# Optimization experiments

Hardware: AMD Instinct MI355X
Metric: run time of the kernel (lower is better)

The kernel has to match this reference:

```python
import jax, jax.numpy as jnp
import numpy as np

# ---- module hyperparameters (from init_kwargs) ----
J = 6      # number of octaves -> subsample by 2**J
Q = 6      # wavelets per octave
T = 16000  # signal length
SUB = 2 ** J           # downsampling factor (=> T_out = 250)
XI_MAX = 0.35          # max center frequency (cycles/sample), kymatio convention


def _build_filters(T, J, Q):
    """Gabor (Morlet-style) band-pass filterbank + Gaussian lowpass, in Fourier domain."""
    freqs = np.fft.fftfreq(T).astype(np.float64)          # (T,) cycles/sample
    n_psi = J * Q
    xis = XI_MAX * 2.0 ** (-np.arange(n_psi) / Q)         # constant-Q center freqs
    r = 2.0 ** (1.0 / Q)
    sigmas = xis * (r - 1.0) / (r + 1.0)                  # constant-Q bandwidths
    psi_hat = np.exp(-((freqs[None, :] - xis[:, None]) ** 2)
                     / (2.0 * sigmas[:, None] ** 2))       # (n_psi, T)
    sigma_phi = XI_MAX / (2.0 ** J)                        # lowpass bandwidth ~ 2^-J
    phi_hat = np.exp(-(freqs ** 2) / (2.0 * sigma_phi ** 2))  # (T,)
    return jnp.asarray(psi_hat, jnp.float32), jnp.asarray(phi_hat, jnp.float32)

PSI_HAT, PHI_HAT = _build_filters(T, J, Q)  # fixed (non-learned) filter constants


def setup_inputs() -> dict:
    key = jax.random.key(0)
    x = jax.random.normal(key, (64, 1, T), dtype=jnp.float32)
    return {"x": x}


def _scattering(x2d):
    """First-order scattering. x2d: (B, T) -> Sx: (B, 1 + J*Q, T//2**J)."""
    X = jnp.fft.fft(x2d, axis=-1)                                   # (B, T) complex
    # order 0: lowpass + subsample
    S0 = jnp.real(jnp.fft.ifft(X * PHI_HAT, axis=-1))[:, ::SUB]     # (B, T')
    # order 1: bandpass -> modulus -> lowpass -> subsample (vectorized over filters)
    U = jnp.abs(jnp.fft.ifft(X[:, None, :] * PSI_HAT[None, :, :], axis=-1))  # (B,JQ,T)
    S1 = jnp.real(jnp.fft.ifft(jnp.fft.fft(U, axis=-1) * PHI_HAT, axis=-1))[:, :, ::SUB]
    return jnp.concatenate([S0[:, None, :], S1], axis=1)            # (B, C, T')


def reference(x):
    # accept (B, T) or (B, 1, T) like the torch module
    if x.ndim == 3:
        x = x[:, 0, :]
    Sx = _scattering(x)[..., None]                                  # (B, C, T', 1)
    C = Sx.shape[1]
    c1 = max(1, C // 3)
    c2 = max(1, 2 * C // 3)
    low = Sx[:, :c1].mean(axis=1)
    mid = Sx[:, c1:c2].mean(axis=1)
    high = Sx[:, c2:].mean(axis=1)
    return jnp.stack([low, mid, high], axis=1)                      # (B, 3, T', 1)
```

## Files before the change

### kernel.cpp

```cpp
#include <hip/hip_runtime.h>
#include <hip/hip_bf16.h>
#include <hip/hip_fp16.h>

#define TLEN 16000
#define NPSI 36
#define NBATCH 64
#define NOUT 250
#define NCH 37
#define DHALF 176
#define KMAX 8000
#define TWO_PI 6.283185307179586

__device__ __forceinline__ int brev7(int q){ return (int)(__brev((unsigned)q) >> 25); }
__device__ __forceinline__ int drev125(int p){
    return (p % 5) * 25 + ((p / 5) % 5) * 5 + (p / 25);
}
__device__ __forceinline__ float lo2f(__half2 v){ return __low2float(v); }
__device__ __forceinline__ float hi2f(__half2 v){ return __high2float(v); }
__device__ __forceinline__ __half2 pk2(float r, float i){
    return __halves2half2(__float2half(r), __float2half(i));
}

__global__ __launch_bounds__(256) void k_ffta(const float* __restrict__ x,
                                              float2* __restrict__ Gtmp){
    __shared__ float xr[16 * 126], xi[16 * 126];
    __shared__ float w125r[125], w125i[125];
    __shared__ float w16r[125],  w16i[125];
    __shared__ float w128r[128], w128i[128];
    const int b = blockIdx.x >> 3, g = blockIdx.x & 7, row0 = 16 * g;
    const int tid = threadIdx.x;

    for (int j = tid; j < 125; j += 256){
        double a = -TWO_PI * (double)j / 125.0;
        w125r[j] = (float)cos(a); w125i[j] = (float)sin(a);
        double a2 = -TWO_PI * (double)j / 16000.0;
        w16r[j] = (float)cos(a2); w16i[j] = (float)sin(a2);
    }
    for (int j = tid; j < 128; j += 256){
        double a = -TWO_PI * (double)j / 128.0;
        w128r[j] = (float)cos(a); w128i[j] = (float)sin(a);
    }
    for (int i = tid; i < 16 * 125; i += 256){
        int n1 = i >> 4, lr = i & 15;
        xr[lr * 126 + n1] = x[b * TLEN + 128 * n1 + row0 + lr];
        xi[lr * 126 + n1] = 0.0f;
    }
    int f = 1;
    for (int s = 25; s >= 1; s /= 5, f *= 5){
        __syncthreads();
        for (int task = tid; task < 25 * 16; task += 256){
            int u = task >> 4, lr = task & 15;
            int blk = u / s, m = u - blk * s;
            int base = lr * 126 + blk * 5 * s + m;
            float vr[5], vi[5];
            #pragma unroll
            for (int r = 0; r < 5; ++r){ vr[r] = xr[base + r * s]; vi[r] = xi[base + r * s]; }
            #pragma unroll
            for (int q = 0; q < 5; ++q){
                float cr = vr[0], ci = vi[0];
                #pragma unroll
                for (int r = 1; r < 5; ++r){
                    int w5 = 25 * ((q * r) % 5);
                    float wr = w125r[w5], wi = w125i[w5];
                    cr += vr[r] * wr - vi[r] * wi;
                    ci += vr[r] * wi + vi[r] * wr;
                }
                int jt = (m * q * f) % 125;
                float tr = w125r[jt], ti = w125i[jt];
                xr[base + q * s] = cr * tr - ci * ti;
                xi[base + q * s] = cr * ti + ci * tr;
            }
        }
    }
    __syncthreads();
    for (int i = tid; i < 125 * 16; i += 256){
        int p = i >> 4, lr = i & 15;
        int n2 = row0 + lr;
        int m = drev125(p);
        int a = m * n2;
        int qq = a / 125, rr = a - qq * 125;
        float tr = w16r[rr] * w128r[qq] - w16i[rr] * w128i[qq];
        float ti = w16r[rr] * w128i[qq] + w16i[rr] * w128r[qq];
        float ar = xr[lr * 126 + p], ai = xi[lr * 126 + p];
        Gtmp[((size_t)b * 125 + p) * 128 + n2] =
            make_float2(ar * tr - ai * ti, ar * ti + ai * tr);
    }
}

__global__ __launch_bounds__(128) void k_fftb(const float2* __restrict__ Gtmp,
                                              float2* __restrict__ Xf){
    __shared__ float gr[128 * 5], gi[128 * 5];
    __shared__ float w128r[128], w128i[128];
    const int b = blockIdx.x / 25, p0 = (blockIdx.x % 25) * 5;
    const int tid = threadIdx.x;
    for (int j = tid; j < 128; j += 128){
        double a = -TWO_PI * (double)j / 128.0;
        w128r[j] = (float)cos(a); w128i[j] = (float)sin(a);
    }
    for (int i = tid; i < 5 * 128; i += 128){
        int ml = i >> 7, n2 = i & 127;
        float2 v = Gtmp[((size_t)b * 125 + p0 + ml) * 128 + n2];
        gr[n2 * 5 + ml] = v.x; gi[n2 * 5 + ml] = v.y;
    }
    for (int span = 64; span >= 1; span >>= 1){
        __syncthreads();
        for (int idx = tid; idx < 320; idx += 128){
            int u = idx / 5, ml = idx - u * 5;
            int blkq = u / span, mm = u % span;
            int i0 = (blkq * 2 * span + mm) * 5 + ml, i1 = i0 + span * 5;
            float ar = gr[i0], ai = gi[i0], br = gr[i1], bi = gi[i1];
            gr[i0] = ar + br; gi[i0] = ai + bi;
            float dr = ar - br, di = ai - bi;
            int jt = mm * (64 / span);
            gr[i1] = dr * w128r[jt] - di * w128i[jt];
            gi[i1] = dr * w128i[jt] + di * w128r[jt];
        }
    }
    __syncthreads();
    for (int idx = tid; idx < 320; idx += 128){
        int u = idx / 5, ml = idx - u * 5;
        int ad = (2 * u) * 5 + ml;
        int k = drev125(p0 + ml) + 125 * brev7(2 * u);
        Xf[(size_t)b * KMAX + k] = make_float2(gr[ad], gi[ad]);
    }
}

template<int P5, int LQ>
__device__ __forceinline__ void env_body(const float2* __restrict__ Xfb,
                                         float* __restrict__ Schan,
                                         int fi, int b, int tid,
                                         __half2* Bc,
                                         float* wPr, float* wPi,
                                         float* wNr, float* wNi,
                                         float* wQr, float* wQi,
                                         float* w5tr, float* w5ti,
                                         float* hfull, int* drevT, float* sred){
    constexpr int Q = 1 << LQ;
    constexpr int N = P5 * Q;
    constexpr int D = TLEN / N;
    constexpr int S1 = P5 / 5;
    constexpr int EPT = (LQ & 1) ? 2 : 4;
    constexpr int NTASK = N / EPT;
    constexpr int NFP = (NTASK + 511) / 512;
    __half* Mag = reinterpret_cast<__half*>(Bc);

    const double xi_d = 0.35 * exp2(-(double)fi / 6.0);
    const double r_d  = exp2(1.0 / 6.0);
    const double sig_d = xi_d * (r_d - 1.0) / (r_d + 1.0);
    const float xi = (float)xi_d;
    const float centerT = (float)(xi_d * (double)TLEN);
    const float sigT = (float)(sig_d * (double)TLEN);
    int klo = (int)floorf(centerT - 5.0f * sigT); if (klo < 1) klo = 1;
    int khi = (int)ceilf(centerT + 5.0f * sigT);  if (khi > KMAX - 1) khi = KMAX - 1;
    const float inv2s2 = (float)(1.0 / (2.0 * sig_d * sig_d));

    for (int j = tid; j < P5; j += 512){
        double a = TWO_PI * (double)j / (double)P5;
        wPr[j] = (float)cos(a); wPi[j] = (float)sin(a);
        double a2 = TWO_PI * (double)j / (double)N;
        wNr[j] = (float)cos(a2); wNi[j] = (float)sin(a2);
        drevT[j] = (P5 == 125) ? drev125(j) : ((j % 5) * 5 + j / 5);
    }
    for (int j = tid; j < Q; j += 512){
        double a = TWO_PI * (double)j / (double)Q;
        wQr[j] = (float)cos(a); wQi[j] = (float)sin(a);
    }
    for (int j = tid; j < 25; j += 512){
        double a = TWO_PI * (double)(((j / 5) * (j % 5)) % 5) / 5.0;
        w5tr[j] = (float)cos(a); w5ti[j] = (float)sin(a);
    }
    for (int j = tid; j <= 2 * DHALF; j += 512){
        double st = 1.0 / (TWO_PI * (0.35 / 64.0));
        double dd = (double)(j - DHALF);
        hfull[j] = (float)((0.35 / 64.0) * sqrt(TWO_PI) * exp(-0.5 * dd * dd / (st * st)));
    }
    __syncthreads();
    for (int task = tid; task < S1 * Q; task += 512){
        int m = task >> LQ, k2 = task & (Q - 1);
        float vr[5], vi[5];
        #pragma unroll
        for (int r = 0; r < 5; ++r){
            int gk = k2 + ((m + r * S1) << LQ);
            float ur = 0.0f, ui = 0.0f;
            if (gk >= klo && gk <= khi){
                float fr = (float)gk * (1.0f / (float)TLEN);
                float d = fr - xi;
                float p = __expf(-d * d * inv2s2) * (1.0f / (float)TLEN);
                float2 Xv = Xfb[gk];
                ur = Xv.x * p; ui = Xv.y * p;
            }
            vr[r] = ur; vi[r] = ui;
        }
        int base = m * Q + k2;
        #pragma unroll
        for (int q = 0; q < 5; ++q){
            float cr = vr[0], ci = vi[0];
            #pragma unroll
            for (int r = 1; r < 5; ++r){
                float wr = w5tr[q * 5 + r], wi = w5ti[q * 5 + r];
                cr += vr[r] * wr - vi[r] * wi;
                ci += vr[r] * wi + vi[r] * wr;
            }
            int jt = m * q;
            float tr = wPr[jt], ti = wPi[jt];
            Bc[base + q * S1 * Q] = pk2(cr * tr - ci * ti, cr * ti + ci * tr);
        }
    }
    if (P5 == 125){
        __syncthreads();
        for (int task = tid; task < 25 * Q; task += 512){
            int u = task >> LQ, k2 = task & (Q - 1);
            int blk = u / 5, m = u - blk * 5;
            int base = (blk * 25 + m) * Q + k2;
            float vr[5], vi[5];
            #pragma unroll
            for (int r = 0; r < 5; ++r){
                __half2 v = Bc[base + r * 5 * Q];
                vr[r] = lo2f(v); vi[r] = hi2f(v);
            }
            #pragma unroll
            for (int q = 0; q < 5; ++q){
                float cr = vr[0], ci = vi[0];
                #pragma unroll
                for (int r = 1; r < 5; ++r){
                    float wr = w5tr[q * 5 + r], wi = w5ti[q * 5 + r];
                    cr += vr[r] * wr - vi[r] * wi;
                    ci += vr[r] * wi + vi[r] * wr;
                }
                int jt = m * q * 5;
                float tr = wPr[jt], ti = wPi[jt];
                Bc[base + q * 5 * Q] = pk2(cr * tr - ci * ti, cr * ti + ci * tr);
            }
        }
    }
    __syncthreads();
    for (int task = tid; task < S1 * Q; task += 512){
        int u = task >> LQ, k2 = task & (Q - 1);
        int base = (u * 5) * Q + k2;
        float vr[5], vi[5];
        #pragma unroll
        for (int r = 0; r < 5; ++r){
            __half2 v = Bc[base + r * Q];
            vr[r] = lo2f(v); vi[r] = hi2f(v);
        }
        #pragma unroll
        for (int q = 0; q < 5; ++q){
            float cr = vr[0], ci = vi[0];
            #pragma unroll
            for (int r = 1; r < 5; ++r){
                float wr = w5tr[q * 5 + r], wi = w5ti[q * 5 + r];
                cr += vr[r] * wr - vi[r] * wi;
                ci += vr[r] * wi + vi[r] * wr;
            }
            int n1 = drevT[5 * u + q];
            int a = k2 * n1;
            int qq = a / P5, rr = a - qq * P5;
            float tr = wQr[qq] * wNr[rr] - wQi[qq] * wNi[rr];
            float ti = wQr[qq] * wNi[rr] + wQi[qq] * wNr[rr];
            Bc[base + q * Q] = pk2(cr * tr - ci * ti, cr * ti + ci * tr);
        }
    }
    #pragma unroll
    for (int pass = 0; pass + 1 < LQ / 2 + (LQ & 1); ++pass){
        const int Sp = Q >> (1 + 2 * pass);
        const int half = Sp >> 1;
        __syncthreads();
        for (int task = tid; task < P5 * (Q / 4); task += 512){
            int prow = task / (Q / 4), v = task & (Q / 4 - 1);
            int blkq = v / half, m = v - blkq * half;
            int base = prow * Q + blkq * 2 * Sp + m;
            __half2 vA = Bc[base],        vB = Bc[base + half];
            __half2 vC = Bc[base + Sp],   vD = Bc[base + Sp + half];
            float Ar = lo2f(vA), Ai = hi2f(vA);
            float B2r = lo2f(vB), B2i = hi2f(vB);
            float Cr = lo2f(vC), Ci = hi2f(vC);
            float D2r = lo2f(vD), D2i = hi2f(vD);
            int jt1 = m * ((Q / 2) / Sp);
            float w1r = wQr[jt1], w1i = wQi[jt1];
            float w2r = wQr[2 * jt1], w2i = wQi[2 * jt1];
            float A1r = Ar + Cr, A1i = Ai + Ci;
            float t1r = Ar - Cr, t1i = Ai - Ci;
            float C1r = t1r * w1r - t1i * w1i, C1i = t1r * w1i + t1i * w1r;
            float B1r = B2r + D2r, B1i = B2i + D2i;
            float t2r = B2r - D2r, t2i = B2i - D2i;
            float t3r = -t2i, t3i = t2r;
            float D1r = t3r * w1r - t3i * w1i, D1i = t3r * w1i + t3i * w1r;
            Bc[base] = pk2(A1r + B1r, A1i + B1i);
            float u1r = A1r - B1r, u1i = A1i - B1i;
            Bc[base + half] = pk2(u1r * w2r - u1i * w2i, u1r * w2i + u1i * w2r);
            Bc[base + Sp] = pk2(C1r + D1r, C1i + D1i);
            float u2r = C1r - D1r, u2i = C1i - D1i;
            Bc[base + Sp + half] = pk2(u2r * w2r - u2i * w2i, u2r * w2i + u2i * w2r);
        }
    }
    __syncthreads();
    float magf[NFP][EPT];
    #pragma unroll
    for (int i = 0; i < NFP; ++i){
        int task = tid + 512 * i;
        if (task < NTASK){
            if (LQ & 1){
                int p = task / (Q / 2), u = task - p * (Q / 2);
                int i0 = p * Q + 2 * u;
                __half2 v0 = Bc[i0], v1 = Bc[i0 + 1];
                float ar = lo2f(v0), ai = hi2f(v0);
                float br2 = lo2f(v1), bi2 = hi2f(v1);
                float o0r = ar + br2, o0i = ai + bi2;
                float o1r = ar - br2, o1i = ai - bi2;
                magf[i][0] = sqrtf(o0r * o0r + o0i * o0i);
                magf[i][1] = sqrtf(o1r * o1r + o1i * o1i);
            } else {
                int prow = task / (Q / 4), v = task & (Q / 4 - 1);
                int base = prow * Q + 4 * v;
                __half2 v0 = Bc[base], v1 = Bc[base + 1];
                __half2 v2 = Bc[base + 2], v3 = Bc[base + 3];
                float Ar = lo2f(v0), Ai = hi2f(v0);
                float B2r = lo2f(v1), B2i = hi2f(v1);
                float Cr = lo2f(v2), Ci = hi2f(v2);
                float D2r = lo2f(v3), D2i = hi2f(v3);
                float A1r = Ar + Cr, A1i = Ai + Ci;
                float C1r = Ar - Cr, C1i = Ai - Ci;
                float B1r = B2r + D2r, B1i = B2i + D2i;
                float t2r = B2r - D2r, t2i = B2i - D2i;
                float D1r = -t2i, D1i = t2r;
                float o0r = A1r + B1r, o0i = A1i + B1i;
                float o1r = A1r - B1r, o1i = A1i - B1i;
                float o2r = C1r + D1r, o2i = C1i + D1i;
                float o3r = C1r - D1r, o3i = C1i - D1i;
                magf[i][0] = sqrtf(o0r * o0r + o0i * o0i);
                magf[i][1] = sqrtf(o1r * o1r + o1i * o1i);
                magf[i][2] = sqrtf(o2r * o2r + o2i * o2i);
                magf[i][3] = sqrtf(o3r * o3r + o3i * o3i);
            }
        }
    }
    __syncthreads();
    #pragma unroll
    for (int i = 0; i < NFP; ++i){
        int task = tid + 512 * i;
        if (task < NTASK){
            int row, s0;
            if (LQ & 1){ row = task / (Q / 2); s0 = 2 * (task - row * (Q / 2)); }
            else       { row = task / (Q / 4); s0 = 4 * (task & (Q / 4 - 1)); }
            #pragma unroll
            for (int e = 0; e < EPT; ++e){
                int slot = s0 + e;
                int n2 = (int)(__brev((unsigned)slot) >> (32 - LQ));
                int np = drevT[row] + P5 * n2;
                Mag[np + (np >> 4)] = __float2half(magf[i][e]);
            }
        }
    }
    __syncthreads();
    float acc = 0.0f;
    if (tid < 500){
        int t = tid - 250 * (tid / 250);
        int q = tid / 250;
        int m0 = 64 * t;
        int lo = m0 - DHALF;
        int nlo = (lo >= 0) ? ((lo + D - 1) / D) : -((-lo) / D);
        int nhi = (m0 + DHALF) / D;
        int n = nlo + q;
        if (n <= nhi){
            int np = n % N; if (np < 0) np += N;
            int d = m0 - D * n + DHALF;
            for (; n <= nhi; n += 2){
                acc += hfull[d] * __half2float(Mag[np + (np >> 4)]);
                d -= 2 * D;
                np += 2; if (np >= N) np -= N;
            }
        }
        sred[tid] = acc;
    }
    __syncthreads();
    if (tid < 250)
        Schan[(b * NCH + 1 + fi) * NOUT + tid] = (sred[tid] + sred[tid + 250]) * (float)D;
}

__global__ __launch_bounds__(512, 4) void k_env_all(const float* __restrict__ x,
                                                    const float2* __restrict__ Xf,
                                                    float* __restrict__ Schan){
    __shared__ __half2 Bc[8000];
    __shared__ float wPr[125], wPi[125];
    __shared__ float wNr[125], wNi[125];
    __shared__ float wQr[128], wQi[128];
    __shared__ float w5tr[25], w5ti[25];
    __shared__ float hfull[2 * DHALF + 1];
    __shared__ int   drevT[125];
    __shared__ float sred[500];

    const int bi = blockIdx.x;
    const int tid = threadIdx.x;
    if (bi < 448){
        int fi = bi >> 6, b = bi & 63;
        env_body<125, 6>(Xf + (size_t)b * KMAX, Schan, fi, b, tid, Bc,
                         wPr, wPi, wNr, wNi, wQr, wQi, w5tr, w5ti, hfull, drevT, sred);
    } else if (bi < 640){
        int t = bi - 448;
        int fi = 7 + (t >> 6), b = t & 63;
        env_body<125, 5>(Xf + (size_t)b * KMAX, Schan, fi, b, tid, Bc,
                         wPr, wPi, wNr, wNi, wQr, wQi, w5tr, w5ti, hfull, drevT, sred);
    } else if (bi < 1088){
        int t = bi - 640;
        int fi = 10 + (t >> 6), b = t & 63;
        env_body<25, 7>(Xf + (size_t)b * KMAX, Schan, fi, b, tid, Bc,
                        wPr, wPi, wNr, wNi, wQr, wQi, w5tr, w5ti, hfull, drevT, sred);
    } else if (bi < 1408){
        int t = bi - 1088;
        int fi = 17 + (t >> 6), b = t & 63;
        env_body<125, 4>(Xf + (size_t)b * KMAX, Schan, fi, b, tid, Bc,
                         wPr, wPi, wNr, wNi, wQr, wQi, w5tr, w5ti, hfull, drevT, sred);
    } else if (bi < 2304){
        int t = bi - 1408;
        int fi = 22 + (t >> 6), b = t & 63;
        env_body<25, 6>(Xf + (size_t)b * KMAX, Schan, fi, b, tid, Bc,
                        wPr, wPi, wNr, wNi, wQr, wQi, w5tr, w5ti, hfull, drevT, sred);
    } else {
        int b = bi - 2304;
        const float* xb = x + (size_t)b * TLEN;
        for (int j = tid; j <= 2 * DHALF; j += 512){
            double st = 1.0 / (TWO_PI * (0.35 / 64.0));
            double dd = (double)(j - DHALF);
            hfull[j] = (float)((0.35 / 64.0) * sqrt(TWO_PI) * exp(-0.5 * dd * dd / (st * st)));
        }
        __syncthreads();
        float acc = 0.0f;
        if (tid < 500){
            int t = tid - 250 * (tid / 250);
            int q = tid / 250;
            int m0 = 64 * t;
            for (int j = q; j <= 2 * DHALF; j += 2){
                int n = m0 - DHALF + j;
                if (n < 0) n += TLEN; else if (n >= TLEN) n -= TLEN;
                acc += hfull[j] * xb[n];
            }
            sred[tid] = acc;
        }
        __syncthreads();
        if (tid < 250)
            Schan[(b * NCH + 0) * NOUT + tid] = sred[tid] + sred[tid + 250];
    }
}

__global__ __launch_bounds__(256) void k_reduce(const float* __restrict__ Schan,
                                                float* __restrict__ out){
    int o = blockIdx.x * 256 + threadIdx.x;
    if (o >= NBATCH * 3 * NOUT) return;
    int b = o / (3 * NOUT);
    int rem = o - b * 3 * NOUT;
    int g = rem / NOUT;
    int t = rem - g * NOUT;
    int c0 = (g == 0) ? 0 : (g == 1 ? 12 : 24);
    int c1 = (g == 0) ? 12 : (g == 1 ? 24 : 37);
    float s = 0.0f;
    for (int c = c0; c < c1; ++c) s += Schan[(b * NCH + c) * NOUT + t];
    out[o] = s / (float)(c1 - c0);
}

__global__ void k_fill_f32(float* out, int n, float v){
    int i = blockIdx.x * 256 + threadIdx.x;
    if (i < n) out[i] = v;
}

extern "C" void kernel_launch(void* const* d_in, const int* in_sizes, int n_in,
                              void* d_out, int out_size, void* d_ws, size_t ws_size,
                              hipStream_t stream) {
    const float* x = (const float*)d_in[0];
    float* out = (float*)d_out;
    const size_t xf_bytes = (size_t)NBATCH * KMAX * sizeof(float2);
    const size_t schan_bytes = (size_t)NBATCH * NCH * NOUT * sizeof(float);
    const size_t gtmp_bytes = (size_t)NBATCH * 16000 * sizeof(float2);
    if (ws_size < xf_bytes + schan_bytes + gtmp_bytes){
        k_fill_f32<<<(out_size + 255) / 256, 256, 0, stream>>>(out, out_size, 800.0f);
        return;
    }
    float2* Xf = (float2*)d_ws;
    float* Schan = (float*)((char*)d_ws + xf_bytes);
    float2* Gtmp = (float2*)((char*)d_ws + xf_bytes + schan_bytes);

    k_ffta<<<NBATCH * 8, 256, 0, stream>>>(x, Gtmp);
    k_fftb<<<NBATCH * 25, 128, 0, stream>>>(Gtmp, Xf);
    k_env_all<<<2368, 512, 0, stream>>>(x, Xf, Schan);
    k_reduce<<<(NBATCH * 3 * NOUT + 255) / 256, 256, 0, stream>>>(Schan, out);
}
```

Measured before the change: 135.1 us.

## Fuse two radix-4 FFT passes into a register-resident radix-16 stage

Replaces the generic loop of shared-memory radix-4 passes in the envelope FFT with a radix-16 stage. Each thread loads 16 half2 elements into registers, runs two radix-4 butterfly layers, then writes them back. For LQ==7 one extra radix-4 pass follows, and smaller sizes use a single hardcoded pass. The aim is fewer LDS reads and writes, fewer __syncthreads barriers and fewer fp16 pack/unpack round trips, at the cost of more registers per thread and less task-level parallelism.

```diff
diff --git a/kernel.cpp b/kernel.cpp
--- a/kernel.cpp
+++ b/kernel.cpp
@@ -124,6 +124,23 @@
         Xf[(size_t)b * KMAX + k] = make_float2(gr[ad], gi[ad]);
     }
 }
+
+#define R4BODY(Ar,Ai,Br_,Bi_,Cr,Ci,Dr,Di,w1r,w1i,w2r,w2i)                   \
+    {                                                                        \
+        float A1r = Ar + Cr, A1i = Ai + Ci;                                  \
+        float t1r = Ar - Cr, t1i = Ai - Ci;                                  \
+        float C1r = t1r * w1r - t1i * w1i, C1i = t1r * w1i + t1i * w1r;      \
+        float B1r = Br_ + Dr, B1i = Bi_ + Di;                                \
+        float t2r = Br_ - Dr, t2i = Bi_ - Di;                                \
+        float t3r = -t2i, t3i = t2r;                                         \
+        float D1r = t3r * w1r - t3i * w1i, D1i = t3r * w1i + t3i * w1r;      \
+        Ar = A1r + B1r; Ai = A1i + B1i;                                      \
+        float u1r = A1r - B1r, u1i = A1i - B1i;                              \
+        Br_ = u1r * w2r - u1i * w2i; Bi_ = u1r * w2i + u1i * w2r;            \
+        Cr = C1r + D1r; Ci = C1i + D1i;                                      \
+        float u2r = C1r - D1r, u2i = C1i - D1i;                              \
+        Dr = u2r * w2r - u2i * w2i; Di = u2r * w2i + u2i * w2r;              \
+    }
 
 template<int P5, int LQ>
 __device__ __forceinline__ void env_body(const float2* __restrict__ Xfb,
@@ -260,37 +277,84 @@
             Bc[base + q * Q] = pk2(cr * tr - ci * ti, cr * ti + ci * tr);
         }
     }
-    #pragma unroll
-    for (int pass = 0; pass + 1 < LQ / 2 + (LQ & 1); ++pass){
-        const int Sp = Q >> (1 + 2 * pass);
-        const int half = Sp >> 1;
+    if (LQ >= 5){
+        constexpr int ST = Q / 16;
+        __syncthreads();
+        for (int task = tid; task < P5 * ST; task += 512){
+            int prow = task / ST, m = task - (task / ST) * ST;
+            int base = prow * Q + m;
+            float er[16], ei[16];
+            #pragma unroll
+            for (int j = 0; j < 16; ++j){
+                __half2 v = Bc[base + j * ST];
+                er[j] = lo2f(v); ei[j] = hi2f(v);
+            }
+            #pragma unroll
+            for (int j0 = 0; j0 < 4; ++j0){
+                int jt1 = m + j0 * ST;
+                float w1r = wQr[jt1], w1i = wQi[jt1];
+                float w2r = wQr[2 * jt1], w2i = wQi[2 * jt1];
+                R4BODY(er[j0], ei[j0], er[j0+4], ei[j0+4],
+                       er[j0+8], ei[j0+8], er[j0+12], ei[j0+12],
+                       w1r, w1i, w2r, w2i)
+            }
+            {
+                int jt1 = 4 * m;
+                float w1r = wQr[jt1], w1i = wQi[jt1];
+                float w2r = wQr[2 * jt1], w2i = wQi[2 * jt1];
+                #pragma unroll
+                for (int k = 0; k < 4; ++k){
+                    R4BODY(er[4*k], ei[4*k], er[4*k+1], ei[4*k+1],
+                           er[4*k+2], ei[4*k+2], er[4*k+3], ei[4*k+3],
+                           w1r, w1i, w2r, w2i)
+                }
+            }
+            #pragma unroll
+            for (int j = 0; j < 16; ++j)
+                Bc[base + j * ST] = pk2(er[j], ei[j]);
+        }
+        if (LQ == 7){
+            __syncthreads();
+            for (int task = tid; task < P5 * (Q / 4); task += 512){
+                int prow = task / (Q / 4), v = task & (Q / 4 - 1);
+                int blkq = v / 2, m = v & 1;
+                int base = prow * Q + blkq * 8 + m;
+                __half2 vA = Bc[base],     vB = Bc[base + 2];
+                __half2 vC = Bc[base + 4], vD = Bc[base + 6];
+                float Ar = lo2f(vA), Ai = hi2f(vA);
+                float B2r = lo2f(vB), B2i = hi2f(vB);
+                float Cr = lo2f(vC), Ci = hi2f(vC);
+                float D2r = lo2f(vD), D2i = hi2f(vD);
+                int jt1 = m * (Q / 8);
+                float w1r = wQr[jt1], w1i = wQi[jt1];
+                float w2r = wQr[2 * jt1], w2i = wQi[2 * jt1];
+                R4BODY(Ar, Ai, B2r, B2i, Cr, Ci, D2r, D2i, w1r, w1i, w2r, w2i)
+                Bc[base] = pk2(Ar, Ai);
+                Bc[base + 2] = pk2(B2r, B2i);
+                Bc[base + 4] = pk2(Cr, Ci);
+                Bc[base + 6] = pk2(D2r, D2i);
+            }
+        }
+    } else {
         __syncthreads();
         for (int task = tid; task < P5 * (Q / 4); task += 512){
             int prow = task / (Q / 4), v = task & (Q / 4 - 1);
-            int blkq = v / half, m = v - blkq * half;
-            int base = prow * Q + blkq * 2 * Sp + m;
-            __half2 vA = Bc[base],        vB = Bc[base + half];
-            __half2 vC = Bc[base + Sp],   vD = Bc[base + Sp + half];
+            int blkq = v / 4, m = v & 3;
+            int base = prow * Q + blkq * 16 + m;
+            __half2 vA = Bc[base],     vB = Bc[base + 4];
+            __half2 vC = Bc[base + 8], vD = Bc[base + 12];
             float Ar = lo2f(vA), Ai = hi2f(vA);
             float B2r = lo2f(vB), B2i = hi2f(vB);
             float Cr = lo2f(vC), Ci = hi2f(vC);
             float D2r = lo2f(vD), D2i = hi2f(vD);
-            int jt1 = m * ((Q / 2) / Sp);
+            int jt1 = m * (Q / 16);
             float w1r = wQr[jt1], w1i = wQi[jt1];
             float w2r = wQr[2 * jt1], w2i = wQi[2 * jt1];
-            float A1r = Ar + Cr, A1i = Ai + Ci;
-            float t1r = Ar - Cr, t1i = Ai - Ci;
-            float C1r = t1r * w1r - t1i * w1i, C1i = t1r * w1i + t1i * w1r;
-            float B1r = B2r + D2r, B1i = B2i + D2i;
-            float t2r = B2r - D2r, t2i = B2i - D2i;
-            float t3r = -t2i, t3i = t2r;
-            float D1r = t3r * w1r - t3i * w1i, D1i = t3r * w1i + t3i * w1r;
-            Bc[base] = pk2(A1r + B1r, A1i + B1i);
-            float u1r = A1r - B1r, u1i = A1i - B1i;
-            Bc[base + half] = pk2(u1r * w2r - u1i * w2i, u1r * w2i + u1i * w2r);
-            Bc[base + Sp] = pk2(C1r + D1r, C1i + D1i);
-            float u2r = C1r - D1r, u2i = C1i - D1i;
-            Bc[base + Sp + half] = pk2(u2r * w2r - u2i * w2i, u2r * w2i + u2i * w2r);
+            R4BODY(Ar, Ai, B2r, B2i, Cr, Ci, D2r, D2i, w1r, w1i, w2r, w2i)
+            Bc[base] = pk2(Ar, Ai);
+            Bc[base + 4] = pk2(B2r, B2i);
+            Bc[base + 8] = pk2(Cr, Ci);
+            Bc[base + 12] = pk2(D2r, D2i);
         }
     }
     __syncthreads();
```

Result: no change. 136.2 us (+0.8%).
